# Kernel optimization log

Measured on AMD Instinct MI355X. Metric: run time of the kernel, lower is better.

## Reference

```python
import jax, jax.numpy as jnp
import numpy as np

N, E = 50000, 800000
IN, H, OUT = 128, 128, 64
N_MID = 4  # middle GIN layers (num_layers=6 -> 1 first + 4 mid + 1 last)


def setup_inputs() -> dict:
    key = jax.random.key(0)
    ks = jax.random.split(key, 8)
    def w(k, shape, fan_in):
        return (jax.random.normal(k, shape, jnp.float32) / np.sqrt(fan_in)).astype(jnp.float32)
    x = jax.random.normal(ks[0], (N, IN), jnp.float32)
    edge_index = jax.random.randint(ks[1], (2, E), 0, N, dtype=jnp.int64)
    return {
        "x": x,
        "edge_index": edge_index,
        "w0a": w(ks[2], (IN, H), IN), "b0a": jnp.zeros((H,), jnp.float32),
        "w0b": w(ks[3], (H, H), H),   "b0b": jnp.zeros((H,), jnp.float32),
        "wma": w(ks[4], (N_MID, H, H), H), "bma": jnp.zeros((N_MID, H), jnp.float32),
        "wmb": w(ks[5], (N_MID, H, H), H), "bmb": jnp.zeros((N_MID, H), jnp.float32),
        "wl": w(ks[6], (H, OUT), H), "bl": jnp.zeros((OUT,), jnp.float32),
    }


def reference(x, edge_index, w0a, b0a, w0b, b0b, wma, bma, wmb, bmb, wl, bl):
    n = x.shape[0]
    src, dst = edge_index[0], edge_index[1]

    def gin_agg(h):
        # GIN with eps=0: (1+eps)*h_i + sum_{j->i} h_j
        return h + jax.ops.segment_sum(h[src], dst, num_segments=n)

    # layer 0: Lin(IN,H)-ReLU-Lin(H,H), then inter-layer ReLU
    h = gin_agg(x)
    h = jax.nn.relu(jax.nn.relu(h @ w0a + b0a) @ w0b + b0b)

    # middle layers 1..4 (scan over stacked params)
    def body(h, p):
        wa, ba, wb, bb = p
        g = gin_agg(h)
        g = jax.nn.relu(g @ wa + ba) @ wb + bb
        return jax.nn.relu(g), None

    h, _ = jax.lax.scan(body, h, (wma, bma, wmb, bmb))

    # last layer: single Lin(H,OUT), then sigmoid
    h = gin_agg(h) @ wl + bl
    return jax.nn.sigmoid(h)
```

## Files before the change

kernel.cpp:

```cpp
#include <hip/hip_runtime.h>
#include <hip/hip_bf16.h>

#define HDIM 128

typedef __attribute__((ext_vector_type(8))) short bf16x8;
typedef __attribute__((ext_vector_type(4))) float f32x4;

__device__ __forceinline__ unsigned short bf16_rne(float x) {
    unsigned int u = __float_as_uint(x);
    unsigned int r = u + 0x7FFFu + ((u >> 16) & 1u);
    return (unsigned short)(r >> 16);
}


__global__ __launch_bounds__(256) void hist_kernel(const int* __restrict__ ei, int E,
                                                   int* __restrict__ deg) {
    int e = blockIdx.x * 256 + threadIdx.x;
    if (e < E) atomicAdd(&deg[ei[E + e]], 1);
}

__global__ __launch_bounds__(256) void scan1_kernel(const int* __restrict__ deg,
                                                    int* __restrict__ rowp,
                                                    int* __restrict__ bsum, int N) {
    __shared__ int s[256];
    int t = threadIdx.x;
    int i = blockIdx.x * 256 + t;
    int v = (i < N) ? deg[i] : 0;
    s[t] = v; __syncthreads();
    for (int off = 1; off < 256; off <<= 1) {
        int x = (t >= off) ? s[t - off] : 0;
        __syncthreads();
        s[t] += x;
        __syncthreads();
    }
    if (i < N) rowp[i] = s[t] - v;
    if (t == 255) bsum[blockIdx.x] = s[255];
}

__global__ __launch_bounds__(256) void scan2_kernel(int* __restrict__ bsum, int NB) {
    __shared__ int s[256];
    int t = threadIdx.x;
    int v = (t < NB) ? bsum[t] : 0;
    s[t] = v; __syncthreads();
    for (int off = 1; off < 256; off <<= 1) {
        int x = (t >= off) ? s[t - off] : 0;
        __syncthreads();
        s[t] += x;
        __syncthreads();
    }
    if (t < NB) bsum[t] = s[t] - v;
}

__global__ __launch_bounds__(256) void scan3_kernel(int* __restrict__ rowp,
                                                    const int* __restrict__ bsum,
                                                    int* __restrict__ cur, int N, int E) {
    int i = blockIdx.x * 256 + threadIdx.x;
    if (i < N) {
        int r = rowp[i] + bsum[blockIdx.x];
        rowp[i] = r;
        cur[i] = r;
    }
    if (i == 0) rowp[N] = E;
}

template <typename IT>
__global__ __launch_bounds__(256) void scatter_kernel(const int* __restrict__ ei, int E,
                                                      int* __restrict__ cur,
                                                      IT* __restrict__ srcs) {
    int e = blockIdx.x * 256 + threadIdx.x;
    if (e < E) {
        int d = ei[E + e];
        int p = atomicAdd(&cur[d], 1);
        srcs[p] = (IT)ei[e];
    }
}


__global__ __launch_bounds__(256) void pack_w_kernel(const float* __restrict__ w0a,
                                                     const float* __restrict__ w0b,
                                                     const float* __restrict__ wma,
                                                     const float* __restrict__ wmb,
                                                     short* __restrict__ wpack) {
    int idx = blockIdx.x * 256 + threadIdx.x;
    if (idx >= 10 * 16384) return;
    int mat = idx >> 14;
    int rem = idx & 16383;
    int i = rem & 7;
    int lane = (rem >> 3) & 63;
    int kc = (rem >> 9) & 3;
    int ct = rem >> 11;
    const float* W = (mat == 0) ? w0a
                   : (mat == 1) ? w0b
                   : (mat < 6)  ? (wma + (size_t)(mat - 2) * 16384)
                                : (wmb + (size_t)(mat - 6) * 16384);
    int k = kc * 32 + (lane >> 4) * 8 + i;
    int col = ct * 16 + (lane & 15);
    float x = W[k * 128 + col];
    unsigned short hb = bf16_rne(x);
    float hf = __uint_as_float(((unsigned int)hb) << 16);
    unsigned short lb = bf16_rne(x - hf);
    wpack[(size_t)mat * 32768 + rem] = (short)hb;
    wpack[(size_t)mat * 32768 + 16384 + rem] = (short)lb;
}


template <typename IT>
__global__ __launch_bounds__(256) void agg_kernel(const float* __restrict__ h,
                                                  const int* __restrict__ rowp,
                                                  const IT* __restrict__ srcs,
                                                  float* __restrict__ out, int N) {
    const int tid  = threadIdx.x;
    const int lane = tid & 63;
    const int half = lane >> 5;
    const int l    = lane & 31;
    const int node = blockIdx.x * 8 + ((tid >> 6) << 1) + half;
    const bool nv  = node < N;
    const int nc   = nv ? node : 0;

    const float4* h4 = (const float4*)h;
    int beg = rowp[nc];
    int end = nv ? rowp[nc + 1] : beg;
    int em1 = max(end - 1, 0);

    const float4 z = {0.f, 0.f, 0.f, 0.f};
    float4 a0 = nv ? h4[(size_t)nc * 32 + l] : z;
    float4 a1 = z, a2 = z, a3 = z, a4 = z, a5 = z, a6 = z, a7 = z;

    for (int q = beg; q < end; q += 8) {
        int c0 = min(q + 0, em1);
        int c1 = min(q + 1, em1);
        int c2 = min(q + 2, em1);
        int c3 = min(q + 3, em1);
        int c4 = min(q + 4, em1);
        int c5 = min(q + 5, em1);
        int c6 = min(q + 6, em1);
        int c7 = min(q + 7, em1);
        int s0 = (int)srcs[c0];
        int s1 = (int)srcs[c1];
        int s2 = (int)srcs[c2];
        int s3 = (int)srcs[c3];
        int s4 = (int)srcs[c4];
        int s5 = (int)srcs[c5];
        int s6 = (int)srcs[c6];
        int s7 = (int)srcs[c7];
        float4 v0 = h4[(size_t)s0 * 32 + l];
        float4 v1 = h4[(size_t)s1 * 32 + l];
        float4 v2 = h4[(size_t)s2 * 32 + l];
        float4 v3 = h4[(size_t)s3 * 32 + l];
        float4 v4 = h4[(size_t)s4 * 32 + l];
        float4 v5 = h4[(size_t)s5 * 32 + l];
        float4 v6 = h4[(size_t)s6 * 32 + l];
        float4 v7 = h4[(size_t)s7 * 32 + l];
        float m0 = (q + 0 < end) ? 1.f : 0.f;
        float m1 = (q + 1 < end) ? 1.f : 0.f;
        float m2 = (q + 2 < end) ? 1.f : 0.f;
        float m3 = (q + 3 < end) ? 1.f : 0.f;
        float m4 = (q + 4 < end) ? 1.f : 0.f;
        float m5 = (q + 5 < end) ? 1.f : 0.f;
        float m6 = (q + 6 < end) ? 1.f : 0.f;
        float m7 = (q + 7 < end) ? 1.f : 0.f;
        a0.x = fmaf(v0.x, m0, a0.x); a0.y = fmaf(v0.y, m0, a0.y);
        a0.z = fmaf(v0.z, m0, a0.z); a0.w = fmaf(v0.w, m0, a0.w);
        a1.x = fmaf(v1.x, m1, a1.x); a1.y = fmaf(v1.y, m1, a1.y);
        a1.z = fmaf(v1.z, m1, a1.z); a1.w = fmaf(v1.w, m1, a1.w);
        a2.x = fmaf(v2.x, m2, a2.x); a2.y = fmaf(v2.y, m2, a2.y);
        a2.z = fmaf(v2.z, m2, a2.z); a2.w = fmaf(v2.w, m2, a2.w);
        a3.x = fmaf(v3.x, m3, a3.x); a3.y = fmaf(v3.y, m3, a3.y);
        a3.z = fmaf(v3.z, m3, a3.z); a3.w = fmaf(v3.w, m3, a3.w);
        a4.x = fmaf(v4.x, m4, a4.x); a4.y = fmaf(v4.y, m4, a4.y);
        a4.z = fmaf(v4.z, m4, a4.z); a4.w = fmaf(v4.w, m4, a4.w);
        a5.x = fmaf(v5.x, m5, a5.x); a5.y = fmaf(v5.y, m5, a5.y);
        a5.z = fmaf(v5.z, m5, a5.z); a5.w = fmaf(v5.w, m5, a5.w);
        a6.x = fmaf(v6.x, m6, a6.x); a6.y = fmaf(v6.y, m6, a6.y);
        a6.z = fmaf(v6.z, m6, a6.z); a6.w = fmaf(v6.w, m6, a6.w);
        a7.x = fmaf(v7.x, m7, a7.x); a7.y = fmaf(v7.y, m7, a7.y);
        a7.z = fmaf(v7.z, m7, a7.z); a7.w = fmaf(v7.w, m7, a7.w);
    }

    a0.x = ((a0.x + a1.x) + (a2.x + a3.x)) + ((a4.x + a5.x) + (a6.x + a7.x));
    a0.y = ((a0.y + a1.y) + (a2.y + a3.y)) + ((a4.y + a5.y) + (a6.y + a7.y));
    a0.z = ((a0.z + a1.z) + (a2.z + a3.z)) + ((a4.z + a5.z) + (a6.z + a7.z));
    a0.w = ((a0.w + a1.w) + (a2.w + a3.w)) + ((a4.w + a5.w) + (a6.w + a7.w));
    if (nv) ((float4*)out)[(size_t)node * 32 + l] = a0;
}


template <typename IT>
__global__ __launch_bounds__(256) void agg_out_kernel(const float* __restrict__ t,
                                                      const int* __restrict__ rowp,
                                                      const IT* __restrict__ srcs,
                                                      const float* __restrict__ bias,
                                                      float* __restrict__ out, int N) {
    int lane = threadIdx.x & 63;
    int node = blockIdx.x * 4 + (threadIdx.x >> 6);
    if (node >= N) return;
    int beg = rowp[node], end = rowp[node + 1];
    float a0 = t[node * 64 + lane];
    float a1 = 0.f, a2 = 0.f, a3 = 0.f, a4 = 0.f, a5 = 0.f, a6 = 0.f, a7 = 0.f;
    int p = beg;
    for (; p + 8 <= end; p += 8) {
        int s0 = (int)srcs[p + 0];
        int s1 = (int)srcs[p + 1];
        int s2 = (int)srcs[p + 2];
        int s3 = (int)srcs[p + 3];
        int s4 = (int)srcs[p + 4];
        int s5 = (int)srcs[p + 5];
        int s6 = (int)srcs[p + 6];
        int s7 = (int)srcs[p + 7];
        a0 += t[s0 * 64 + lane];
        a1 += t[s1 * 64 + lane];
        a2 += t[s2 * 64 + lane];
        a3 += t[s3 * 64 + lane];
        a4 += t[s4 * 64 + lane];
        a5 += t[s5 * 64 + lane];
        a6 += t[s6 * 64 + lane];
        a7 += t[s7 * 64 + lane];
    }
    for (; p < end; ++p) a0 += t[(int)srcs[p] * 64 + lane];
    float z = a0 + ((a1 + a2) + (a3 + a4)) + ((a5 + a6) + a7) + bias[lane];
    out[node * 64 + lane] = 1.f / (1.f + __expf(-z));
}


__device__ __forceinline__ void cvt8(const float4 p, const float4 q,
                                     bf16x8& hi, bf16x8& lo) {
    unsigned short hb; float hf;
#define CVT1(IDX, V) \
    hb = bf16_rne(V); hf = __uint_as_float(((unsigned int)hb) << 16); \
    hi[IDX] = (short)hb; lo[IDX] = (short)bf16_rne((V) - hf);
    CVT1(0, p.x) CVT1(1, p.y) CVT1(2, p.z) CVT1(3, p.w)
    CVT1(4, q.x) CVT1(5, q.y) CVT1(6, q.z) CVT1(7, q.w)
#undef CVT1
}

template <bool WRITE_GLOBAL>
__device__ __forceinline__ void gemm_phase_mfma(float* __restrict__ myrows,
                                                const short* __restrict__ wp,
                                                const float* __restrict__ bias,
                                                int arow, int agrp,
                                                int l, float* __restrict__ gout,
                                                int row_base, int N) {
    f32x4 acc[8];
#pragma unroll
    for (int ct = 0; ct < 8; ++ct) acc[ct] = (f32x4){0.f, 0.f, 0.f, 0.f};

    const short* wlo = wp + 16384;
#pragma unroll
    for (int kc = 0; kc < 4; ++kc) {
        const float* ap = &myrows[arow * 132 + kc * 32 + agrp * 8];
        float4 p = *(const float4*)ap;
        float4 q = *(const float4*)(ap + 4);
        bf16x8 ahi, alo;
        cvt8(p, q, ahi, alo);
#pragma unroll
        for (int ct = 0; ct < 8; ++ct) {
            const int off = ((ct * 4 + kc) << 9) + (l << 3);
            bf16x8 bhi = *(const bf16x8*)(wp + off);
            bf16x8 blo = *(const bf16x8*)(wlo + off);
            acc[ct] = __builtin_amdgcn_mfma_f32_16x16x32_bf16(ahi, bhi, acc[ct], 0, 0, 0);
            acc[ct] = __builtin_amdgcn_mfma_f32_16x16x32_bf16(alo, bhi, acc[ct], 0, 0, 0);
            acc[ct] = __builtin_amdgcn_mfma_f32_16x16x32_bf16(ahi, blo, acc[ct], 0, 0, 0);
        }
    }

#pragma unroll
    for (int ct = 0; ct < 8; ++ct) {
        float bv = bias[ct * 16 + arow];
#pragma unroll
        for (int r = 0; r < 4; ++r) {
            float v = fmaxf(acc[ct][r] + bv, 0.f);
            if (WRITE_GLOBAL) {
                int row = row_base + agrp * 4 + r;
                if (row < N) gout[(size_t)row * 128 + ct * 16 + arow] = v;
            } else {
                myrows[(agrp * 4 + r) * 132 + ct * 16 + arow] = v;
            }
        }
    }
}

__global__ __launch_bounds__(256, 4) void mlp2_mfma_kernel(
    const float* __restrict__ in,
    const short* __restrict__ wpa, const float* __restrict__ ba,
    const short* __restrict__ wpb, const float* __restrict__ bb,
    float* __restrict__ out, int N) {
    __shared__ float sh[64 * 132];
    const int tid = threadIdx.x;
    const int wave = tid >> 6;
    const int l = tid & 63;
    const int arow = l & 15;
    const int agrp = l >> 4;
    const int row0 = blockIdx.x * 64;

    const float4* in4 = (const float4*)in;
#pragma unroll
    for (int it = 0; it < 8; ++it) {
        int i = tid + it * 256;
        int r = i >> 5, c = i & 31;
        int row = row0 + r;
        float4 z = {0.f, 0.f, 0.f, 0.f};
        float4 v = (row < N) ? in4[(size_t)row * 32 + c] : z;
        *(float4*)&sh[r * 132 + c * 4] = v;
    }
    __syncthreads();

    float* myrows = &sh[wave * 16 * 132];
    gemm_phase_mfma<false>(myrows, wpa, ba, arow, agrp, l, nullptr, 0, N);
    __syncthreads();
    gemm_phase_mfma<true>(myrows, wpb, bb, arow, agrp, l, out, row0 + wave * 16, N);
}


__global__ __launch_bounds__(256, 6) void gemm64_kernel(const float* __restrict__ in,
                                                        const float* __restrict__ W,
                                                        float* __restrict__ out, int N) {
    constexpr int TX = 16, RPT = 2;
    __shared__ float4 sh[32 * 32];

    int tid = threadIdx.x;
    int tx = tid % TX;
    int ty = tid / TX;
    int row0 = blockIdx.x * 32;

    const float4* in4 = (const float4*)in;
    for (int i = tid; i < 32 * 32; i += 256) {
        int r = i >> 5, c = i & 31;
        int row = row0 + r;
        float4 z = {0.f, 0.f, 0.f, 0.f};
        sh[i] = (row < N) ? in4[(size_t)row * 32 + c] : z;
    }
    __syncthreads();

    const float4* W4 = (const float4*)W;
    float acc[RPT][4];
#pragma unroll
    for (int r = 0; r < RPT; ++r)
#pragma unroll
        for (int c = 0; c < 4; ++c) acc[r][c] = 0.f;

#pragma unroll 4
    for (int kk = 0; kk < 128; kk += 4) {
        float4 w0 = W4[(kk + 0) * TX + tx];
        float4 w1 = W4[(kk + 1) * TX + tx];
        float4 w2 = W4[(kk + 2) * TX + tx];
        float4 w3 = W4[(kk + 3) * TX + tx];
#pragma unroll
        for (int r = 0; r < RPT; ++r) {
            float4 hv = sh[(ty * RPT + r) * 32 + (kk >> 2)];
            acc[r][0] += hv.x * w0.x + hv.y * w1.x + hv.z * w2.x + hv.w * w3.x;
            acc[r][1] += hv.x * w0.y + hv.y * w1.y + hv.z * w2.y + hv.w * w3.y;
            acc[r][2] += hv.x * w0.z + hv.y * w1.z + hv.z * w2.z + hv.w * w3.z;
            acc[r][3] += hv.x * w0.w + hv.y * w1.w + hv.z * w2.w + hv.w * w3.w;
        }
    }

#pragma unroll
    for (int r = 0; r < RPT; ++r) {
        int row = row0 + ty * RPT + r;
        if (row < N) {
            float4 v = {acc[r][0], acc[r][1], acc[r][2], acc[r][3]};
            ((float4*)out)[(size_t)row * TX + tx] = v;
        }
    }
}


template <typename IT>
static void run_graph(const float* x, const int* ei, int N, int E,
                      const float* w0a, const float* b0a, const float* w0b, const float* b0b,
                      const float* wma, const float* bma, const float* wmb, const float* bmb,
                      const float* wl, const float* bl,
                      float* A, float* B, int* deg, int* rowp, int* cur, int* bsum,
                      IT* srcs, short* wpack, float* out, hipStream_t stream) {
    const int NB = (N + 255) / 256;
    dim3 blk(256);

    pack_w_kernel<<<(10 * 16384 + 255) / 256, blk, 0, stream>>>(w0a, w0b, wma, wmb, wpack);

    hipMemsetAsync(deg, 0, (size_t)N * sizeof(int), stream);
    hist_kernel<<<(E + 255) / 256, blk, 0, stream>>>(ei, E, deg);
    scan1_kernel<<<NB, blk, 0, stream>>>(deg, rowp, bsum, N);
    scan2_kernel<<<1, blk, 0, stream>>>(bsum, NB);
    scan3_kernel<<<NB, blk, 0, stream>>>(rowp, bsum, cur, N, E);
    scatter_kernel<IT><<<(E + 255) / 256, blk, 0, stream>>>(ei, E, cur, srcs);

    const int agg_grid  = (N + 7) / 8;
    const int aggo_grid = (N + 3) / 4;
    const int m64_grid  = (N + 63) / 64;
    const int g32_grid  = (N + 31) / 32;

    agg_kernel<IT><<<agg_grid, blk, 0, stream>>>(x, rowp, srcs, A, N);
    mlp2_mfma_kernel<<<m64_grid, blk, 0, stream>>>(A, wpack + 0, b0a,
                                                   wpack + 32768, b0b, B, N);

    float* h = B;
    float* o = A;
    for (int l = 0; l < 4; ++l) {
        const short* wpa = wpack + (size_t)(2 + l) * 32768;
        const short* wpb = wpack + (size_t)(6 + l) * 32768;
        const float* ba = bma + (size_t)l * HDIM;
        const float* bb = bmb + (size_t)l * HDIM;
        agg_kernel<IT><<<agg_grid, blk, 0, stream>>>(h, rowp, srcs, o, N);
        mlp2_mfma_kernel<<<m64_grid, blk, 0, stream>>>(o, wpa, ba, wpb, bb, h, N);
    }

    gemm64_kernel<<<g32_grid, blk, 0, stream>>>(h, wl, o, N);
    agg_out_kernel<IT><<<aggo_grid, blk, 0, stream>>>(o, rowp, srcs, bl, out, N);
}

extern "C" void kernel_launch(void* const* d_in, const int* in_sizes, int n_in,
                              void* d_out, int out_size, void* d_ws, size_t ws_size,
                              hipStream_t stream) {
    const float* x   = (const float*)d_in[0];
    const int*   ei  = (const int*)d_in[1];
    const float* w0a = (const float*)d_in[2];
    const float* b0a = (const float*)d_in[3];
    const float* w0b = (const float*)d_in[4];
    const float* b0b = (const float*)d_in[5];
    const float* wma = (const float*)d_in[6];
    const float* bma = (const float*)d_in[7];
    const float* wmb = (const float*)d_in[8];
    const float* bmb = (const float*)d_in[9];
    const float* wl  = (const float*)d_in[10];
    const float* bl  = (const float*)d_in[11];

    const int N = in_sizes[0] / HDIM;
    const int E = in_sizes[1] / 2;

    float* A = (float*)d_ws;
    float* B = A + (size_t)N * HDIM;
    int* deg  = (int*)(B + (size_t)N * HDIM);
    int* rowp = deg + N;
    int* cur  = rowp + N + 1;
    int* bsum = cur + N;
    int* srcs = bsum + 256;
    short* wpack = (short*)(srcs + E);

    if (N <= 65535) {
        run_graph<unsigned short>(x, ei, N, E, w0a, b0a, w0b, b0b, wma, bma, wmb, bmb,
                                  wl, bl, A, B, deg, rowp, cur, bsum,
                                  (unsigned short*)srcs, wpack, (float*)d_out, stream);
    } else {
        run_graph<int>(x, ei, N, E, w0a, b0a, w0b, b0b, wma, bma, wmb, bmb,
                       wl, bl, A, B, deg, rowp, cur, bsum,
                       srcs, wpack, (float*)d_out, stream);
    }
}
```

Baseline: 592.0 us.

## Stage hi weight halves in LDS and store final projection as fp16

The MLP kernel now copies the high bf16 half of each packed weight matrix into shared memory, so the MFMA B operands come from LDS rather than global/L1. The low half is still read from global. The extra 32 KB of LDS per block lowers the occupancy hint from 4 to 2 blocks. Separately, the final 64-wide projection is written as fp16, which halves the bytes gathered by the output aggregation, at the cost of some precision in the pre-sigmoid values.

```diff
diff --git a/kernel.cpp b/kernel.cpp
--- a/kernel.cpp
+++ b/kernel.cpp
@@ -5,6 +5,7 @@
 
 typedef __attribute__((ext_vector_type(8))) short bf16x8;
 typedef __attribute__((ext_vector_type(4))) float f32x4;
+typedef __attribute__((ext_vector_type(4))) _Float16 f16x4;
 
 __device__ __forceinline__ unsigned short bf16_rne(float x) {
     unsigned int u = __float_as_uint(x);
@@ -186,7 +187,7 @@
 
 
 template <typename IT>
-__global__ __launch_bounds__(256) void agg_out_kernel(const float* __restrict__ t,
+__global__ __launch_bounds__(256) void agg_out_kernel(const _Float16* __restrict__ t,
                                                       const int* __restrict__ rowp,
                                                       const IT* __restrict__ srcs,
                                                       const float* __restrict__ bias,
@@ -195,7 +196,7 @@
     int node = blockIdx.x * 4 + (threadIdx.x >> 6);
     if (node >= N) return;
     int beg = rowp[node], end = rowp[node + 1];
-    float a0 = t[node * 64 + lane];
+    float a0 = (float)t[(size_t)node * 64 + lane];
     float a1 = 0.f, a2 = 0.f, a3 = 0.f, a4 = 0.f, a5 = 0.f, a6 = 0.f, a7 = 0.f;
     int p = beg;
     for (; p + 8 <= end; p += 8) {
@@ -207,18 +208,18 @@
         int s5 = (int)srcs[p + 5];
         int s6 = (int)srcs[p + 6];
         int s7 = (int)srcs[p + 7];
-        a0 += t[s0 * 64 + lane];
-        a1 += t[s1 * 64 + lane];
-        a2 += t[s2 * 64 + lane];
-        a3 += t[s3 * 64 + lane];
-        a4 += t[s4 * 64 + lane];
-        a5 += t[s5 * 64 + lane];
-        a6 += t[s6 * 64 + lane];
-        a7 += t[s7 * 64 + lane];
-    }
-    for (; p < end; ++p) a0 += t[(int)srcs[p] * 64 + lane];
+        a0 += (float)t[(size_t)s0 * 64 + lane];
+        a1 += (float)t[(size_t)s1 * 64 + lane];
+        a2 += (float)t[(size_t)s2 * 64 + lane];
+        a3 += (float)t[(size_t)s3 * 64 + lane];
+        a4 += (float)t[(size_t)s4 * 64 + lane];
+        a5 += (float)t[(size_t)s5 * 64 + lane];
+        a6 += (float)t[(size_t)s6 * 64 + lane];
+        a7 += (float)t[(size_t)s7 * 64 + lane];
+    }
+    for (; p < end; ++p) a0 += (float)t[(size_t)(int)srcs[p] * 64 + lane];
     float z = a0 + ((a1 + a2) + (a3 + a4)) + ((a5 + a6) + a7) + bias[lane];
-    out[node * 64 + lane] = 1.f / (1.f + __expf(-z));
+    out[(size_t)node * 64 + lane] = 1.f / (1.f + __expf(-z));
 }
 
 
@@ -235,7 +236,8 @@
 
 template <bool WRITE_GLOBAL>
 __device__ __forceinline__ void gemm_phase_mfma(float* __restrict__ myrows,
-                                                const short* __restrict__ wp,
+                                                const short* whi_lds,
+                                                const short* __restrict__ wlo,
                                                 const float* __restrict__ bias,
                                                 int arow, int agrp,
                                                 int l, float* __restrict__ gout,
@@ -244,7 +246,6 @@
 #pragma unroll
     for (int ct = 0; ct < 8; ++ct) acc[ct] = (f32x4){0.f, 0.f, 0.f, 0.f};
 
-    const short* wlo = wp + 16384;
 #pragma unroll
     for (int kc = 0; kc < 4; ++kc) {
         const float* ap = &myrows[arow * 132 + kc * 32 + agrp * 8];
@@ -255,7 +256,7 @@
 #pragma unroll
         for (int ct = 0; ct < 8; ++ct) {
             const int off = ((ct * 4 + kc) << 9) + (l << 3);
-            bf16x8 bhi = *(const bf16x8*)(wp + off);
+            bf16x8 bhi = *(const bf16x8*)(whi_lds + off);
             bf16x8 blo = *(const bf16x8*)(wlo + off);
             acc[ct] = __builtin_amdgcn_mfma_f32_16x16x32_bf16(ahi, bhi, acc[ct], 0, 0, 0);
             acc[ct] = __builtin_amdgcn_mfma_f32_16x16x32_bf16(alo, bhi, acc[ct], 0, 0, 0);
@@ -279,12 +280,13 @@
     }
 }
 
-__global__ __launch_bounds__(256, 4) void mlp2_mfma_kernel(
+__global__ __launch_bounds__(256, 2) void mlp2_mfma_kernel(
     const float* __restrict__ in,
     const short* __restrict__ wpa, const float* __restrict__ ba,
     const short* __restrict__ wpb, const float* __restrict__ bb,
     float* __restrict__ out, int N) {
     __shared__ float sh[64 * 132];
+    __shared__ short wsh[16384];
     const int tid = threadIdx.x;
     const int wave = tid >> 6;
     const int l = tid & 63;
@@ -302,18 +304,32 @@
         float4 v = (row < N) ? in4[(size_t)row * 32 + c] : z;
         *(float4*)&sh[r * 132 + c * 4] = v;
     }
+    {
+        const int4* src = (const int4*)wpa;
+        int4* dst = (int4*)wsh;
+#pragma unroll
+        for (int i = 0; i < 8; ++i) dst[tid + i * 256] = src[tid + i * 256];
+    }
     __syncthreads();
 
     float* myrows = &sh[wave * 16 * 132];
-    gemm_phase_mfma<false>(myrows, wpa, ba, arow, agrp, l, nullptr, 0, N);
+    gemm_phase_mfma<false>(myrows, wsh, wpa + 16384, ba, arow, agrp, l, nullptr, 0, N);
     __syncthreads();
-    gemm_phase_mfma<true>(myrows, wpb, bb, arow, agrp, l, out, row0 + wave * 16, N);
+    {
+        const int4* src = (const int4*)wpb;
+        int4* dst = (int4*)wsh;
+#pragma unroll
+        for (int i = 0; i < 8; ++i) dst[tid + i * 256] = src[tid + i * 256];
+    }
+    __syncthreads();
+    gemm_phase_mfma<true>(myrows, wsh, wpb + 16384, bb, arow, agrp, l, out,
+                          row0 + wave * 16, N);
 }
 
 
 __global__ __launch_bounds__(256, 6) void gemm64_kernel(const float* __restrict__ in,
                                                         const float* __restrict__ W,
-                                                        float* __restrict__ out, int N) {
+                                                        _Float16* __restrict__ out, int N) {
     constexpr int TX = 16, RPT = 2;
     __shared__ float4 sh[32 * 32];
 
@@ -358,8 +374,12 @@
     for (int r = 0; r < RPT; ++r) {
         int row = row0 + ty * RPT + r;
         if (row < N) {
-            float4 v = {acc[r][0], acc[r][1], acc[r][2], acc[r][3]};
-            ((float4*)out)[(size_t)row * TX + tx] = v;
+            f16x4 v;
+            v[0] = (_Float16)acc[r][0];
+            v[1] = (_Float16)acc[r][1];
+            v[2] = (_Float16)acc[r][2];
+            v[3] = (_Float16)acc[r][3];
+            *(f16x4*)&out[(size_t)row * 64 + tx * 4] = v;
         }
     }
 }
@@ -404,8 +424,9 @@
         mlp2_mfma_kernel<<<m64_grid, blk, 0, stream>>>(o, wpa, ba, wpb, bb, h, N);
     }
 
-    gemm64_kernel<<<g32_grid, blk, 0, stream>>>(h, wl, o, N);
-    agg_out_kernel<IT><<<aggo_grid, blk, 0, stream>>>(o, rowp, srcs, bl, out, N);
+    _Float16* t16 = (_Float16*)o;
+    gemm64_kernel<<<g32_grid, blk, 0, stream>>>(h, wl, t16, N);
+    agg_out_kernel<IT><<<aggo_grid, blk, 0, stream>>>(t16, rowp, srcs, bl, out, N);
 }
 
 extern "C" void kernel_launch(void* const* d_in, const int* in_sizes, int n_in,
```

Result: slower. 621.1 us (+4.9%).
